# Kernel tuning notes

Hardware: AMD Instinct MI355X
Metric: run time of the kernel (lower is better)

## Reference

```python
import jax, jax.numpy as jnp
import numpy as np

B, T, C, H = 2, 2048, 1024, 16
D = C // H

def setup_inputs() -> dict:
    key = jax.random.key(0)
    ks = jax.random.split(key, 8)
    s = 1.0 / np.sqrt(C)
    return {
        "x": jax.random.normal(ks[0], (B, T, C), dtype=jnp.float32),
        "Wk": jax.random.normal(ks[1], (C, C), dtype=jnp.float32) * s,
        "Wq": jax.random.normal(ks[2], (C, C), dtype=jnp.float32) * s,
        "bq": jax.random.normal(ks[3], (C,), dtype=jnp.float32) * 0.02,
        "Wv": jax.random.normal(ks[4], (C, C), dtype=jnp.float32) * s,
        "bv": jax.random.normal(ks[5], (C,), dtype=jnp.float32) * 0.02,
        "Wo": jax.random.normal(ks[6], (C, C), dtype=jnp.float32) * s,
        "bo": jax.random.normal(ks[7], (C,), dtype=jnp.float32) * 0.02,
    }

def reference(x, Wk, Wq, bq, Wv, bv, Wo, bo):
    b, t, c = x.shape
    # projections (key has no bias, matching nn.Linear(bias=False))
    q = (x @ Wq.T + bq).reshape(b, t, H, D).transpose(0, 2, 1, 3)  # [B,H,T,D]
    k = (x @ Wk.T).reshape(b, t, H, D).transpose(0, 2, 1, 3)
    v = (x @ Wv.T + bv).reshape(b, t, H, D).transpose(0, 2, 1, 3)
    scale = D ** -0.5
    attn = jnp.einsum('bhqd,bhkd->bhqk', q, k) * scale  # [B,H,T,T]
    causal = jnp.tril(jnp.ones((t, t), dtype=bool))
    attn = jnp.where(causal[None, None], attn, -jnp.inf)
    attn = jax.nn.softmax(attn, axis=-1)
    y = jnp.einsum('bhqk,bhkd->bhqd', attn, v)  # [B,H,T,D]
    y = y.transpose(0, 2, 1, 3).reshape(b, t, c)
    return y @ Wo.T + bo
```

## Files before the change

kernel.cpp:

```cpp
#include <hip/hip_runtime.h>
#include <hip/hip_bf16.h>
#include <stdint.h>

#define B_ 2
#define T_ 2048
#define C_ 1024
#define H_ 16
#define D_ 64
#define M_ (B_ * T_)

typedef __bf16 bf16x8 __attribute__((ext_vector_type(8)));
typedef float f32x4 __attribute__((ext_vector_type(4)));
typedef float f32x16 __attribute__((ext_vector_type(16)));

__device__ inline void gload_lds16(const void* g, void* l) {
  __builtin_amdgcn_global_load_lds(
      (const __attribute__((address_space(1))) void*)g,
      (__attribute__((address_space(3))) void*)l, 16, 0, 0);
}

__global__ __launch_bounds__(256) void cvt_all(
    const float* __restrict__ x, const float* __restrict__ Wq,
    const float* __restrict__ Wk, const float* __restrict__ Wv,
    const float* __restrict__ Wo, __hip_bfloat16* __restrict__ xb,
    __hip_bfloat16* __restrict__ wqb, __hip_bfloat16* __restrict__ wkb,
    __hip_bfloat16* __restrict__ wvb, __hip_bfloat16* __restrict__ wob) {
  size_t t = (size_t)blockIdx.x * 256 + threadIdx.x;
  size_t e = t * 4;
  const float* src;
  __hip_bfloat16* dst;
  size_t off;
  if (e < 4194304) {
    src = x; dst = xb; off = e;
  } else {
    size_t u = e - 4194304;
    int seg = (int)(u >> 20);
    off = u & 1048575;
    src = (seg == 0) ? Wq : (seg == 1) ? Wk : (seg == 2) ? Wv : Wo;
    dst = (seg == 0) ? wqb : (seg == 1) ? wkb : (seg == 2) ? wvb : wob;
  }
  float4 v = *(const float4*)(src + off);
  union { __hip_bfloat16 h[4]; ushort4 u4; } cv;
  cv.h[0] = __float2bfloat16(v.x);
  cv.h[1] = __float2bfloat16(v.y);
  cv.h[2] = __float2bfloat16(v.z);
  cv.h[3] = __float2bfloat16(v.w);
  *(ushort4*)(dst + off) = cv.u4;
}

__global__ __launch_bounds__(256) void gemm_qkv(
    const __hip_bfloat16* __restrict__ X,
    const __hip_bfloat16* __restrict__ Wq,
    const __hip_bfloat16* __restrict__ Wk,
    const __hip_bfloat16* __restrict__ Wv,
    const float* __restrict__ bq, const float* __restrict__ bv,
    __hip_bfloat16* __restrict__ Qo, __hip_bfloat16* __restrict__ Ko,
    __hip_bfloat16* __restrict__ VTo) {
  const int z = blockIdx.z;
  const int bx = ((blockIdx.x & 3) << 3) | (blockIdx.x >> 2);
  const __hip_bfloat16* Amat;
  const __hip_bfloat16* Bmat;
  int bm, bn;
  if (z == 2) {
    Amat = Wv; Bmat = X; bm = blockIdx.y; bn = bx;
  } else {
    Amat = X; Bmat = (z == 0) ? Wq : Wk; bm = bx; bn = blockIdx.y;
  }

  const int tid = threadIdx.x;
  const int w = tid >> 6, lane = tid & 63;
  const int wr = w >> 1, wc = w & 1;
  const int lrow = lane & 15, lk = (lane >> 4) * 8;

  __shared__ __hip_bfloat16 As[128 * 32];
  __shared__ __hip_bfloat16 Bs[128 * 32];

  f32x4 acc[4][4];
#pragma unroll
  for (int m = 0; m < 4; ++m)
#pragma unroll
    for (int n = 0; n < 4; ++n) acc[m][n] = (f32x4){0.f, 0.f, 0.f, 0.f};

  for (int k0 = 0; k0 < C_; k0 += 32) {
#pragma unroll
    for (int it = 0; it < 2; ++it) {
      int e = it * 2048 + w * 512 + lane * 8;
      int row = e >> 5, col = e & 31;
      gload_lds16(Amat + (size_t)(bm * 128 + row) * C_ + k0 + col, &As[e]);
      gload_lds16(Bmat + (size_t)(bn * 128 + row) * C_ + k0 + col, &Bs[e]);
    }
    asm volatile("s_waitcnt vmcnt(0)" ::: "memory");
    __syncthreads();

    bf16x8 af[4], bfr[4];
#pragma unroll
    for (int m = 0; m < 4; ++m)
      af[m] = *(const bf16x8*)&As[(wr * 64 + m * 16 + lrow) * 32 + lk];
#pragma unroll
    for (int n = 0; n < 4; ++n)
      bfr[n] = *(const bf16x8*)&Bs[(wc * 64 + n * 16 + lrow) * 32 + lk];
#pragma unroll
    for (int m = 0; m < 4; ++m)
#pragma unroll
      for (int n = 0; n < 4; ++n)
        acc[m][n] = __builtin_amdgcn_mfma_f32_16x16x32_bf16(af[m], bfr[n],
                                                            acc[m][n], 0, 0, 0);
    __syncthreads();
  }

#pragma unroll
  for (int m = 0; m < 4; ++m) {
#pragma unroll
    for (int n = 0; n < 4; ++n) {
      f32x4 v = acc[m][n];
      int rowm = bm * 128 + wr * 64 + m * 16 + (lane >> 4) * 4;
      int coln = bn * 128 + wc * 64 + n * 16 + (lane & 15);
      if (z == 2) {
        int b = coln >> 11, tl = coln & 2047;
#pragma unroll
        for (int r = 0; r < 4; ++r) {
          int rc = rowm + r;
          int h = rc >> 6, d = rc & 63;
          VTo[(((size_t)(b * H_ + h)) * D_ + d) * T_ + tl] =
              __float2bfloat16(v[r] + bv[rc]);
        }
      } else {
        float bb = (z == 0) ? bq[coln] : 0.f;
        float sc = (z == 0) ? 0.18033688011112042f : 1.0f;
        int h = coln >> 6, d = coln & 63;
        __hip_bfloat16* Out = (z == 0) ? Qo : Ko;
#pragma unroll
        for (int r = 0; r < 4; ++r) {
          int row = rowm + r;
          int b = row >> 11, t = row & 2047;
          Out[(((size_t)(b * H_ + h)) * T_ + t) * D_ + d] =
              __float2bfloat16((v[r] + bb) * sc);
        }
      }
    }
  }
}

__global__ __launch_bounds__(256) void gemm_out(
    const __hip_bfloat16* __restrict__ X,
    const __hip_bfloat16* __restrict__ W,
    const float* __restrict__ bias, float* __restrict__ Out) {
  const int bm = ((blockIdx.x & 3) << 3) | (blockIdx.x >> 2);
  const int bn = blockIdx.y;
  const int tid = threadIdx.x;
  const int w = tid >> 6, lane = tid & 63;
  const int wr = w >> 1, wc = w & 1;
  const int lrow = lane & 15, lk = (lane >> 4) * 8;

  __shared__ __hip_bfloat16 As[128 * 32];
  __shared__ __hip_bfloat16 Bs[64 * 32];

  f32x4 acc[4][2];
#pragma unroll
  for (int m = 0; m < 4; ++m)
#pragma unroll
    for (int n = 0; n < 2; ++n) acc[m][n] = (f32x4){0.f, 0.f, 0.f, 0.f};

  for (int k0 = 0; k0 < C_; k0 += 32) {
#pragma unroll
    for (int it = 0; it < 2; ++it) {
      int e = it * 2048 + tid * 8;
      int row = e >> 5, col = e & 31;
      gload_lds16(X + (size_t)(bm * 128 + row) * C_ + k0 + col, &As[e]);
    }
    {
      int e = tid * 8;
      int row = e >> 5, col = e & 31;
      gload_lds16(W + (size_t)(bn * 64 + row) * C_ + k0 + col, &Bs[e]);
    }
    asm volatile("s_waitcnt vmcnt(0)" ::: "memory");
    __syncthreads();

    bf16x8 af[4], bfr[2];
#pragma unroll
    for (int m = 0; m < 4; ++m)
      af[m] = *(const bf16x8*)&As[(wr * 64 + m * 16 + lrow) * 32 + lk];
#pragma unroll
    for (int n = 0; n < 2; ++n)
      bfr[n] = *(const bf16x8*)&Bs[(wc * 32 + n * 16 + lrow) * 32 + lk];
#pragma unroll
    for (int m = 0; m < 4; ++m)
#pragma unroll
      for (int n = 0; n < 2; ++n)
        acc[m][n] = __builtin_amdgcn_mfma_f32_16x16x32_bf16(af[m], bfr[n],
                                                            acc[m][n], 0, 0, 0);
    __syncthreads();
  }

#pragma unroll
  for (int m = 0; m < 4; ++m) {
#pragma unroll
    for (int n = 0; n < 2; ++n) {
      f32x4 v = acc[m][n];
      int coln = bn * 64 + wc * 32 + n * 16 + (lane & 15);
      float bb = bias[coln];
#pragma unroll
      for (int r = 0; r < 4; ++r) {
        int row = bm * 128 + wr * 64 + m * 16 + (lane >> 4) * 4 + r;
        Out[(size_t)row * C_ + coln] = v[r] + bb;
      }
    }
  }
}

#define MASKV_ -1e30f

__global__ __launch_bounds__(512, 4) void attn_fwd(
    const __hip_bfloat16* __restrict__ Q, const __hip_bfloat16* __restrict__ K,
    const __hip_bfloat16* __restrict__ VT, __hip_bfloat16* __restrict__ Y) {
  const int bid = blockIdx.x;
  const int qt = 15 - (bid >> 5);
  const int bh = bid & 31;
  const int tid = threadIdx.x;
  const int wid = tid >> 6, lane = tid & 63;
  const int g = wid >> 2, wq = wid & 3;
  const int hi = lane >> 5, q32 = lane & 31;
  const size_t base = (size_t)bh * T_ * D_;
  const int b = bh >> 4, hh = bh & 15;

  __shared__ __align__(16) char smem[65536 + 1024];
  auto Ks = (__hip_bfloat16(*)[2][64][64])(smem);
  auto Vts = (__hip_bfloat16(*)[2][64][64])(smem + 32768);
  float* Sml = (float*)(smem + 65536);
  float(*Om)[32][68] = (float(*)[32][68])(smem);

  const int gt = tid & 255;
  const int srow = gt >> 3, scnk = gt & 7;
  const int swz = (scnk ^ (srow & 7)) * 8;

#define STAGE(buf, kt)                                                      \
  {                                                                         \
    _Pragma("unroll") for (int h2 = 0; h2 < 2; ++h2) {                      \
      int row = srow + 32 * h2;                                             \
      gload_lds16(K + base + (size_t)((kt)*64 + row) * D_ + swz,            \
                  &Ks[g][(buf)][row][scnk * 8]);                            \
      gload_lds16(VT + base + (size_t)row * T_ + (kt)*64 + swz,             \
                  &Vts[g][(buf)][row][scnk * 8]);                           \
    }                                                                       \
  }

  const int qg = qt * 128 + wq * 32 + q32;

  bf16x8 qf[4];
#pragma unroll
  for (int dk = 0; dk < 4; ++dk)
    qf[dk] = *(const bf16x8*)&Q[base + (size_t)qg * D_ + dk * 16 + hi * 8];

  f32x16 o0 = {}, o1 = {};
  float l_run = 0.f;

  STAGE(0, g);
  asm volatile("s_waitcnt vmcnt(0)" ::: "memory");
  __syncthreads();

  for (int s = 0; s <= qt; ++s) {
    const int kt = 2 * s + g;
    const int cur = s & 1;
    if (s < qt) STAGE(cur ^ 1, 2 * (s + 1) + g);

    f32x16 st0 = {}, st1 = {};
    __builtin_amdgcn_s_setprio(1);
#pragma unroll
    for (int dk = 0; dk < 4; ++dk) {
      int off = (dk * 16 + hi * 8) ^ ((lane & 7) << 3);
      bf16x8 a0 = *(const bf16x8*)&Ks[g][cur][q32][off];
      bf16x8 a1 = *(const bf16x8*)&Ks[g][cur][q32 + 32][off];
      st0 = __builtin_amdgcn_mfma_f32_32x32x16_bf16(a0, qf[dk], st0, 0, 0, 0);
      st1 = __builtin_amdgcn_mfma_f32_32x32x16_bf16(a1, qf[dk], st1, 0, 0, 0);
    }
    __builtin_amdgcn_s_setprio(0);

    float sc[32];
#pragma unroll
    for (int r = 0; r < 16; ++r) {
      sc[r] = st0[r];
      sc[16 + r] = st1[r];
    }
    if (s == qt) {
#pragma unroll
      for (int r = 0; r < 16; ++r) {
        int kvl = (r & 3) + 8 * (r >> 2) + 4 * hi;
        if (kt * 64 + kvl > qg) sc[r] = MASKV_;
        if (kt * 64 + 32 + kvl > qg) sc[16 + r] = MASKV_;
      }
    }
#pragma unroll
    for (int r = 0; r < 32; ++r) sc[r] = __builtin_exp2f(sc[r]);
    float ts[16];
#pragma unroll
    for (int r = 0; r < 16; ++r) ts[r] = sc[r] + sc[16 + r];
#pragma unroll
    for (int off2 = 8; off2 > 0; off2 >>= 1)
#pragma unroll
      for (int r = 0; r < 8; ++r)
        if (r < off2) ts[r] = ts[r] + ts[r + off2];
    float ls = ts[0];
    ls += __shfl_xor(ls, 32);
    l_run += ls;

    __builtin_amdgcn_s_setprio(1);
#pragma unroll
    for (int ks = 0; ks < 4; ++ks) {
      union { unsigned w[4]; bf16x8 v; } pa;
      unsigned A, Bb;
      asm("v_cvt_pk_bf16_f32 %0, %1, %2"
          : "=v"(A) : "v"(sc[ks * 8 + 0]), "v"(sc[ks * 8 + 1]));
      asm("v_cvt_pk_bf16_f32 %0, %1, %2"
          : "=v"(Bb) : "v"(sc[ks * 8 + 4]), "v"(sc[ks * 8 + 5]));
      asm volatile("v_permlane32_swap_b32 %0, %1" : "+v"(A), "+v"(Bb));
      pa.w[0] = A;
      pa.w[2] = Bb;
      asm("v_cvt_pk_bf16_f32 %0, %1, %2"
          : "=v"(A) : "v"(sc[ks * 8 + 2]), "v"(sc[ks * 8 + 3]));
      asm("v_cvt_pk_bf16_f32 %0, %1, %2"
          : "=v"(Bb) : "v"(sc[ks * 8 + 6]), "v"(sc[ks * 8 + 7]));
      asm volatile("v_permlane32_swap_b32 %0, %1" : "+v"(A), "+v"(Bb));
      pa.w[1] = A;
      pa.w[3] = Bb;

      int voff = (ks * 16 + hi * 8) ^ ((lane & 7) << 3);
      bf16x8 v0 = *(const bf16x8*)&Vts[g][cur][q32][voff];
      bf16x8 v1 = *(const bf16x8*)&Vts[g][cur][q32 + 32][voff];
      o0 = __builtin_amdgcn_mfma_f32_32x32x16_bf16(v0, pa.v, o0, 0, 0, 0);
      o1 = __builtin_amdgcn_mfma_f32_32x32x16_bf16(v1, pa.v, o1, 0, 0, 0);
    }
    __builtin_amdgcn_s_setprio(0);

    asm volatile("s_waitcnt vmcnt(0)" ::: "memory");
    __syncthreads();
  }

  if (lane < 32) Sml[(g * 4 + wq) * 32 + lane] = l_run;
  __syncthreads();
  float lstar = l_run + Sml[((1 - g) * 4 + wq) * 32 + q32];

  if (g == 1) {
#pragma unroll
    for (int dt = 0; dt < 2; ++dt) {
#pragma unroll
      for (int grp = 0; grp < 4; ++grp) {
        int dbase = grp * 8 + hi * 4 + dt * 32;
        float4 t4;
        t4.x = (dt ? o1[grp * 4 + 0] : o0[grp * 4 + 0]);
        t4.y = (dt ? o1[grp * 4 + 1] : o0[grp * 4 + 1]);
        t4.z = (dt ? o1[grp * 4 + 2] : o0[grp * 4 + 2]);
        t4.w = (dt ? o1[grp * 4 + 3] : o0[grp * 4 + 3]);
        *(float4*)&Om[wq][q32][dbase] = t4;
      }
    }
  }
  __syncthreads();
  if (g == 0) {
    float inv = 1.0f / lstar;
#pragma unroll
    for (int dt = 0; dt < 2; ++dt) {
#pragma unroll
      for (int grp = 0; grp < 4; ++grp) {
        int dbase = grp * 8 + hi * 4 + dt * 32;
        float4 m4 = *(float4*)&Om[wq][q32][dbase];
        union { __hip_bfloat16 h4[4]; ushort4 u; } pk;
        float e0 = (dt ? o1[grp * 4 + 0] : o0[grp * 4 + 0]) + m4.x;
        float e1 = (dt ? o1[grp * 4 + 1] : o0[grp * 4 + 1]) + m4.y;
        float e2 = (dt ? o1[grp * 4 + 2] : o0[grp * 4 + 2]) + m4.z;
        float e3 = (dt ? o1[grp * 4 + 3] : o0[grp * 4 + 3]) + m4.w;
        pk.h4[0] = __float2bfloat16(e0 * inv);
        pk.h4[1] = __float2bfloat16(e1 * inv);
        pk.h4[2] = __float2bfloat16(e2 * inv);
        pk.h4[3] = __float2bfloat16(e3 * inv);
        *(ushort4*)&Y[((size_t)b * T_ + qg) * C_ + hh * 64 + dbase] = pk.u;
      }
    }
  }
}

extern "C" void kernel_launch(void* const* d_in, const int* in_sizes, int n_in,
                              void* d_out, int out_size, void* d_ws,
                              size_t ws_size, hipStream_t stream) {
  const float* x = (const float*)d_in[0];
  const float* Wk = (const float*)d_in[1];
  const float* Wq = (const float*)d_in[2];
  const float* bq = (const float*)d_in[3];
  const float* Wv = (const float*)d_in[4];
  const float* bv = (const float*)d_in[5];
  const float* Wo = (const float*)d_in[6];
  const float* bo = (const float*)d_in[7];
  float* out = (float*)d_out;

  char* ws = (char*)d_ws;
  __hip_bfloat16* xb = (__hip_bfloat16*)(ws);
  __hip_bfloat16* wqb = (__hip_bfloat16*)(ws + (8ull << 20));
  __hip_bfloat16* wkb = (__hip_bfloat16*)(ws + (10ull << 20));
  __hip_bfloat16* wvb = (__hip_bfloat16*)(ws + (12ull << 20));
  __hip_bfloat16* wob = (__hip_bfloat16*)(ws + (14ull << 20));
  __hip_bfloat16* Qb = (__hip_bfloat16*)(ws + (16ull << 20));
  __hip_bfloat16* Kb = (__hip_bfloat16*)(ws + (24ull << 20));
  __hip_bfloat16* VTb = (__hip_bfloat16*)(ws + (32ull << 20));
  __hip_bfloat16* Yb = (__hip_bfloat16*)(ws + (40ull << 20));

  cvt_all<<<8192, 256, 0, stream>>>(x, Wq, Wk, Wv, Wo, xb, wqb, wkb, wvb, wob);
  gemm_qkv<<<dim3(32, 8, 3), 256, 0, stream>>>(xb, wqb, wkb, wvb, bq, bv, Qb,
                                               Kb, VTb);
  attn_fwd<<<512, 512, 0, stream>>>(Qb, Kb, VTb, Yb);
  gemm_out<<<dim3(32, 16), 256, 0, stream>>>(Yb, wob, bo, out);
}
```

Baseline: 105.5 us.

## Split attention KV range across separate blocks and merge partials in new kernel

The 512-thread attention block that split the KV range between two wave groups inside one block is replaced by two independent 256-thread blocks per query tile. Each writes unnormalized bf16 partial outputs and row sums to scratch (the output buffer and the start of the workspace). A new merge kernel sums the partials, normalizes and writes Y. This targets better scheduling and occupancy from smaller blocks. It costs an extra launch, extra global traffic for the partials, and an extra bf16 rounding of the partial sums.

```diff
diff --git a/kernel.cpp b/kernel.cpp
--- a/kernel.cpp
+++ b/kernel.cpp
@@ -210,27 +210,24 @@
 
 #define MASKV_ -1e30f
 
-__global__ __launch_bounds__(512, 4) void attn_fwd(
+__global__ __launch_bounds__(256, 4) void attn_part(
     const __hip_bfloat16* __restrict__ Q, const __hip_bfloat16* __restrict__ K,
-    const __hip_bfloat16* __restrict__ VT, __hip_bfloat16* __restrict__ Y) {
+    const __hip_bfloat16* __restrict__ VT, __hip_bfloat16* __restrict__ OP,
+    float* __restrict__ lpart) {
   const int bid = blockIdx.x;
-  const int qt = 15 - (bid >> 5);
+  const int qt = 15 - (bid >> 6);
+  const int sp = (bid >> 5) & 1;
   const int bh = bid & 31;
   const int tid = threadIdx.x;
-  const int wid = tid >> 6, lane = tid & 63;
-  const int g = wid >> 2, wq = wid & 3;
+  const int wq = tid >> 6, lane = tid & 63;
   const int hi = lane >> 5, q32 = lane & 31;
   const size_t base = (size_t)bh * T_ * D_;
-  const int b = bh >> 4, hh = bh & 15;
-
-  __shared__ __align__(16) char smem[65536 + 1024];
-  auto Ks = (__hip_bfloat16(*)[2][64][64])(smem);
-  auto Vts = (__hip_bfloat16(*)[2][64][64])(smem + 32768);
-  float* Sml = (float*)(smem + 65536);
-  float(*Om)[32][68] = (float(*)[32][68])(smem);
-
-  const int gt = tid & 255;
-  const int srow = gt >> 3, scnk = gt & 7;
+  const int tileIdx = qt * 32 + bh;
+
+  __shared__ __hip_bfloat16 Ks[2][64][64];
+  __shared__ __hip_bfloat16 Vts[2][64][64];
+
+  const int srow = tid >> 3, scnk = tid & 7;
   const int swz = (scnk ^ (srow & 7)) * 8;
 
 #define STAGE(buf, kt)                                                      \
@@ -238,9 +235,9 @@
     _Pragma("unroll") for (int h2 = 0; h2 < 2; ++h2) {                      \
       int row = srow + 32 * h2;                                             \
       gload_lds16(K + base + (size_t)((kt)*64 + row) * D_ + swz,            \
-                  &Ks[g][(buf)][row][scnk * 8]);                            \
+                  &Ks[(buf)][row][scnk * 8]);                               \
       gload_lds16(VT + base + (size_t)row * T_ + (kt)*64 + swz,             \
-                  &Vts[g][(buf)][row][scnk * 8]);                           \
+                  &Vts[(buf)][row][scnk * 8]);                              \
     }                                                                       \
   }
 
@@ -254,22 +251,22 @@
   f32x16 o0 = {}, o1 = {};
   float l_run = 0.f;
 
-  STAGE(0, g);
+  STAGE(0, sp);
   asm volatile("s_waitcnt vmcnt(0)" ::: "memory");
   __syncthreads();
 
   for (int s = 0; s <= qt; ++s) {
-    const int kt = 2 * s + g;
+    const int kt = 2 * s + sp;
     const int cur = s & 1;
-    if (s < qt) STAGE(cur ^ 1, 2 * (s + 1) + g);
+    if (s < qt) STAGE(cur ^ 1, 2 * (s + 1) + sp);
 
     f32x16 st0 = {}, st1 = {};
     __builtin_amdgcn_s_setprio(1);
 #pragma unroll
     for (int dk = 0; dk < 4; ++dk) {
       int off = (dk * 16 + hi * 8) ^ ((lane & 7) << 3);
-      bf16x8 a0 = *(const bf16x8*)&Ks[g][cur][q32][off];
-      bf16x8 a1 = *(const bf16x8*)&Ks[g][cur][q32 + 32][off];
+      bf16x8 a0 = *(const bf16x8*)&Ks[cur][q32][off];
+      bf16x8 a1 = *(const bf16x8*)&Ks[cur][q32 + 32][off];
       st0 = __builtin_amdgcn_mfma_f32_32x32x16_bf16(a0, qf[dk], st0, 0, 0, 0);
       st1 = __builtin_amdgcn_mfma_f32_32x32x16_bf16(a1, qf[dk], st1, 0, 0, 0);
     }
@@ -324,8 +321,8 @@
       pa.w[3] = Bb;
 
       int voff = (ks * 16 + hi * 8) ^ ((lane & 7) << 3);
-      bf16x8 v0 = *(const bf16x8*)&Vts[g][cur][q32][voff];
-      bf16x8 v1 = *(const bf16x8*)&Vts[g][cur][q32 + 32][voff];
+      bf16x8 v0 = *(const bf16x8*)&Vts[cur][q32][voff];
+      bf16x8 v1 = *(const bf16x8*)&Vts[cur][q32 + 32][voff];
       o0 = __builtin_amdgcn_mfma_f32_32x32x16_bf16(v0, pa.v, o0, 0, 0, 0);
       o1 = __builtin_amdgcn_mfma_f32_32x32x16_bf16(v1, pa.v, o1, 0, 0, 0);
     }
@@ -335,47 +332,59 @@
     __syncthreads();
   }
 
-  if (lane < 32) Sml[(g * 4 + wq) * 32 + lane] = l_run;
-  __syncthreads();
-  float lstar = l_run + Sml[((1 - g) * 4 + wq) * 32 + q32];
-
-  if (g == 1) {
-#pragma unroll
-    for (int dt = 0; dt < 2; ++dt) {
-#pragma unroll
-      for (int grp = 0; grp < 4; ++grp) {
-        int dbase = grp * 8 + hi * 4 + dt * 32;
-        float4 t4;
-        t4.x = (dt ? o1[grp * 4 + 0] : o0[grp * 4 + 0]);
-        t4.y = (dt ? o1[grp * 4 + 1] : o0[grp * 4 + 1]);
-        t4.z = (dt ? o1[grp * 4 + 2] : o0[grp * 4 + 2]);
-        t4.w = (dt ? o1[grp * 4 + 3] : o0[grp * 4 + 3]);
-        *(float4*)&Om[wq][q32][dbase] = t4;
-      }
-    }
-  }
-  __syncthreads();
-  if (g == 0) {
-    float inv = 1.0f / lstar;
-#pragma unroll
-    for (int dt = 0; dt < 2; ++dt) {
-#pragma unroll
-      for (int grp = 0; grp < 4; ++grp) {
-        int dbase = grp * 8 + hi * 4 + dt * 32;
-        float4 m4 = *(float4*)&Om[wq][q32][dbase];
-        union { __hip_bfloat16 h4[4]; ushort4 u; } pk;
-        float e0 = (dt ? o1[grp * 4 + 0] : o0[grp * 4 + 0]) + m4.x;
-        float e1 = (dt ? o1[grp * 4 + 1] : o0[grp * 4 + 1]) + m4.y;
-        float e2 = (dt ? o1[grp * 4 + 2] : o0[grp * 4 + 2]) + m4.z;
-        float e3 = (dt ? o1[grp * 4 + 3] : o0[grp * 4 + 3]) + m4.w;
-        pk.h4[0] = __float2bfloat16(e0 * inv);
-        pk.h4[1] = __float2bfloat16(e1 * inv);
-        pk.h4[2] = __float2bfloat16(e2 * inv);
-        pk.h4[3] = __float2bfloat16(e3 * inv);
-        *(ushort4*)&Y[((size_t)b * T_ + qg) * C_ + hh * 64 + dbase] = pk.u;
-      }
-    }
-  }
+  const size_t obase = ((size_t)(sp * 512 + tileIdx) * 128 + wq * 32 + q32) * 64;
+#pragma unroll
+  for (int dt = 0; dt < 2; ++dt) {
+#pragma unroll
+    for (int grp = 0; grp < 4; ++grp) {
+      int dbase = grp * 8 + hi * 4 + dt * 32;
+      union { __hip_bfloat16 h4[4]; ushort4 u; } pk;
+      pk.h4[0] = __float2bfloat16(dt ? o1[grp * 4 + 0] : o0[grp * 4 + 0]);
+      pk.h4[1] = __float2bfloat16(dt ? o1[grp * 4 + 1] : o0[grp * 4 + 1]);
+      pk.h4[2] = __float2bfloat16(dt ? o1[grp * 4 + 2] : o0[grp * 4 + 2]);
+      pk.h4[3] = __float2bfloat16(dt ? o1[grp * 4 + 3] : o0[grp * 4 + 3]);
+      *(ushort4*)&OP[obase + dbase] = pk.u;
+    }
+  }
+  if (lane < 32)
+    lpart[(size_t)(sp * 512 + tileIdx) * 128 + wq * 32 + lane] = l_run;
+}
+
+__global__ __launch_bounds__(256) void attn_merge(
+    const __hip_bfloat16* __restrict__ OP, const float* __restrict__ lpart,
+    __hip_bfloat16* __restrict__ Y) {
+  int tg = blockIdx.x * 256 + threadIdx.x;
+  int tileIdx = tg >> 10;
+  int rem = tg & 1023;
+  int row = rem >> 3, chunk = rem & 7;
+  int qt = tileIdx >> 5, bh = tileIdx & 31;
+  int b = bh >> 4, hh = bh & 15;
+  size_t i0 = ((size_t)tileIdx * 128 + row) * 64 + chunk * 8;
+  size_t i1 = ((size_t)(512 + tileIdx) * 128 + row) * 64 + chunk * 8;
+  float l = lpart[(size_t)tileIdx * 128 + row] +
+            lpart[(size_t)(512 + tileIdx) * 128 + row];
+  float inv = 1.0f / l;
+  ushort4 a0 = *(const ushort4*)&OP[i0];
+  ushort4 a1 = *(const ushort4*)&OP[i0 + 4];
+  ushort4 b0 = *(const ushort4*)&OP[i1];
+  ushort4 b1 = *(const ushort4*)&OP[i1 + 4];
+  union { __hip_bfloat16 h[8]; ushort4 u[2]; } out;
+  const unsigned short* pa = (const unsigned short*)&a0;
+  const unsigned short* pb = (const unsigned short*)&b0;
+#pragma unroll
+  for (int j = 0; j < 8; ++j) {
+    unsigned ua = ((j < 4 ? ((const unsigned short*)&a0)[j]
+                          : ((const unsigned short*)&a1)[j - 4]));
+    unsigned ub = ((j < 4 ? ((const unsigned short*)&b0)[j]
+                          : ((const unsigned short*)&b1)[j - 4]));
+    float fa = __uint_as_float(ua << 16);
+    float fb = __uint_as_float(ub << 16);
+    out.h[j] = __float2bfloat16((fa + fb) * inv);
+  }
+  (void)pa; (void)pb;
+  size_t ybase = ((size_t)b * T_ + qt * 128 + row) * C_ + hh * 64 + chunk * 8;
+  *(ushort4*)&Y[ybase] = out.u[0];
+  *(ushort4*)&Y[ybase + 4] = out.u[1];
 }
 
 extern "C" void kernel_launch(void* const* d_in, const int* in_sizes, int n_in,
@@ -401,10 +410,13 @@
   __hip_bfloat16* Kb = (__hip_bfloat16*)(ws + (24ull << 20));
   __hip_bfloat16* VTb = (__hip_bfloat16*)(ws + (32ull << 20));
   __hip_bfloat16* Yb = (__hip_bfloat16*)(ws + (40ull << 20));
+  __hip_bfloat16* OP = (__hip_bfloat16*)d_out;
+  float* lpart = (float*)(ws);
 
   cvt_all<<<8192, 256, 0, stream>>>(x, Wq, Wk, Wv, Wo, xb, wqb, wkb, wvb, wob);
   gemm_qkv<<<dim3(32, 8, 3), 256, 0, stream>>>(xb, wqb, wkb, wvb, bq, bv, Qb,
                                                Kb, VTb);
-  attn_fwd<<<512, 512, 0, stream>>>(Qb, Kb, VTb, Yb);
+  attn_part<<<1024, 256, 0, stream>>>(Qb, Kb, VTb, OP, lpart);
+  attn_merge<<<2048, 256, 0, stream>>>(OP, lpart, Yb);
   gemm_out<<<dim3(32, 16), 256, 0, stream>>>(Yb, wob, bo, out);
 }
```

Measured after the change: 106.7 us. About the same (+1.1%).
